# Kernel optimization log

Measured on AMD Instinct MI355X. Metric: run time of the kernel, lower is better.

## Reference

```python
import jax, jax.numpy as jnp
import numpy as np

K_LEN, I_LEN, DIM = 1024, 8192, 128


def setup_inputs() -> dict:
    key = jax.random.key(0)
    k1, k2 = jax.random.split(key)
    kernel = jax.random.normal(k1, (K_LEN, DIM), dtype=jnp.float32)
    x = jax.random.normal(k2, (I_LEN, DIM), dtype=jnp.float32)
    return {"kernel": kernel, "x": x}


def _cost_matrix(kernel, x):
    # squared Euclidean pairwise distances, (K, I), via GEMM form
    k2 = jnp.sum(kernel * kernel, axis=-1)  # (K,)
    x2 = jnp.sum(x * x, axis=-1)            # (I,)
    c = k2[:, None] + x2[None, :] - 2.0 * (kernel @ x.T)
    return jnp.maximum(c, 0.0)


def _acc_matrix(c):
    # DTW DP: D[i,j] = c[i,j] + min(D[i-1,j-1], D[i-1,j], D[i,j-1])
    # Row recurrence solved per-row with a (min,+) prefix scan:
    #   e[j] = min(D_prev[j-1], D_prev[j]) + c[j]   (e[0] = D_prev[0] + c[0])
    #   D[j] = S[j] + cummin(e - S),  S = cumsum(c_row)
    row0 = jnp.cumsum(c[0])

    def step(prev, c_row):
        m = jnp.concatenate([prev[:1], jnp.minimum(prev[:-1], prev[1:])])
        e = m + c_row
        S = jnp.cumsum(c_row)
        row = S + jax.lax.cummin(e - S)
        return row, row

    _, rows = jax.lax.scan(step, row0, c[1:])
    return jnp.concatenate([row0[None, :], rows], axis=0)  # (K, I)


def _backtrack(D):
    # tslearn-style backtracking from (K-1, I-1) to (0, 0).
    # Candidate order [diag, up, left]; argmin ties pick first (diag),
    # matching numpy.argmin used by tslearn. Out-of-range -> +inf border.
    K, I = D.shape
    Dp = jnp.full((K + 1, I + 1), jnp.inf, dtype=D.dtype).at[1:, 1:].set(D)
    L = K + I - 1  # max possible path length

    def step(carry, _):
        k, i, fin = carry
        emit = (k, i, jnp.logical_not(fin))
        fin2 = fin | ((k == 0) & (i == 0))
        cand = jnp.stack([Dp[k, i], Dp[k, i + 1], Dp[k + 1, i]])
        a = jnp.argmin(cand)
        nk = jnp.where(fin2, k, k - (a != 2).astype(k.dtype))
        ni = jnp.where(fin2, i, i - (a != 1).astype(i.dtype))
        return (nk, ni, fin2), emit

    init = (jnp.int32(K - 1), jnp.int32(I - 1), jnp.bool_(False))
    _, (ks, iss, valid) = jax.lax.scan(step, init, None, length=L)
    return ks, iss, valid


def reference(kernel, x):
    # Path search uses detached tensors in the original module.
    c = jax.lax.stop_gradient(_cost_matrix(kernel, x))
    D = _acc_matrix(c)
    ks, iss, valid = _backtrack(D)
    # sum of squared diffs along the optimal alignment path (gather + reduce)
    d2 = jnp.sum((kernel[ks] - x[iss]) ** 2, axis=-1)  # (L,)
    return jnp.sum(jnp.where(valid, d2, 0.0))
```

## Files before the change

### kernel.cpp

```cpp
#include <hip/hip_runtime.h>
#include <hip/hip_bf16.h>

typedef unsigned short ushort_t;
typedef unsigned int uint_t;

#define KL 1024
#define IL 8192
#define DIMV 128
#define NS 16
#define NB 258
#define NIT2 270
#define SSH (8256*64)
#define GATE 416
#define INF __builtin_inff()

typedef __attribute__((ext_vector_type(8))) short v8s;
typedef __attribute__((ext_vector_type(4))) float v4f;

__global__ __launch_bounds__(256) void knorms(
    const float* __restrict__ kern, const float* __restrict__ xx,
    float* __restrict__ x2, float* __restrict__ k2, int* __restrict__ flags) {
  if (blockIdx.x == 0 && threadIdx.x < NS) flags[threadIdx.x] = 0;
  const int lane = threadIdx.x & 63;
  const int row = blockIdx.x * 4 + (threadIdx.x >> 6);
  const float* src;
  float* dst;
  if (row < IL) { src = xx + (size_t)row * DIMV; dst = x2 + row; }
  else          { src = kern + (size_t)(row - IL) * DIMV; dst = k2 + (row - IL); }
  float2 v = *(const float2*)(src + lane * 2);
  float ss = v.x * v.x + v.y * v.y;
  #pragma unroll
  for (int off = 32; off > 0; off >>= 1) ss += __shfl_down(ss, off, 64);
  if (lane == 0) *dst = ss;
}

__device__ __forceinline__ v8s pack_bf16x8(float4 a, float4 b) {
  union { unsigned int u[4]; v8s v; } r;
  union { __hip_bfloat162 h; unsigned int u; } t;
  t.h = __float22bfloat162_rn(make_float2(a.x, a.y)); r.u[0] = t.u;
  t.h = __float22bfloat162_rn(make_float2(a.z, a.w)); r.u[1] = t.u;
  t.h = __float22bfloat162_rn(make_float2(b.x, b.y)); r.u[2] = t.u;
  t.h = __float22bfloat162_rn(make_float2(b.z, b.w)); r.u[3] = t.u;
  return r.v;
}

__global__ __launch_bounds__(256) void kgemm(
    const float* __restrict__ kern, const float* __restrict__ xx,
    const float* __restrict__ x2, const float* __restrict__ k2,
    ushort_t* __restrict__ c_h) {
  __shared__ float ctile[64 * 64];
  const int T = threadIdx.x;
  const int w = T >> 6;
  const int lane = T & 63;
  const int lo = lane & 15;
  const int hi = lane >> 4;
  const int i0 = blockIdx.x * 64;
  const int s  = blockIdx.y;
  const int kr0 = s * 64;

  v4f acc[4] = {};
  #pragma unroll
  for (int ks = 0; ks < 4; ks++) {
    const int k = ks * 32 + hi * 8;
    const float* bp = xx + (size_t)(i0 + w * 16 + lo) * DIMV + k;
    v8s bf = pack_bf16x8(*(const float4*)bp, *(const float4*)(bp + 4));
    #pragma unroll
    for (int rt = 0; rt < 4; rt++) {
      const float* ap = kern + (size_t)(kr0 + rt * 16 + lo) * DIMV + k;
      v8s af = pack_bf16x8(*(const float4*)ap, *(const float4*)(ap + 4));
      acc[rt] = __builtin_amdgcn_mfma_f32_16x16x32_bf16(af, bf, acc[rt], 0, 0, 0);
    }
  }
  const float x2v = x2[i0 + w * 16 + lo];
  const int n_local = w * 16 + lo;
  #pragma unroll
  for (int rt = 0; rt < 4; rt++) {
    float4 k2f = *(const float4*)&k2[kr0 + rt * 16 + hi * 4];
    #pragma unroll
    for (int q = 0; q < 4; q++) {
      const int m_local = rt * 16 + hi * 4 + q;
      float cval = fmaxf((&k2f.x)[q] + x2v - 2.f * acc[rt][q], 0.f);
      ctile[n_local * 64 + ((m_local + 2 * n_local) & 63)] = cval;
    }
  }
  __syncthreads();
  _Float16* ob = (_Float16*)(c_h + (size_t)s * SSH);
  #pragma unroll
  for (int q = 0; q < 32; q++) {
    int tt = w + q * 4;
    int di = tt - lane;
    if (tt <= 126 && di >= 0 && di < 64) {
      int t = i0 + tt;
      int tp = t >> 1;
      ob[(((size_t)(tp >> 4) * 1024) + lane * 16 + (tp & 15)) * 2 + (t & 1)] =
          (_Float16)ctile[di * 64 + ((lane + 2 * di) & 63)];
    }
  }
}

__device__ __forceinline__ float dpp_wave_shr1(float oldv, float src) {
  return __int_as_float(__builtin_amdgcn_update_dpp(
      __float_as_int(oldv), __float_as_int(src), 0x138, 0xF, 0xF, false));
}

__global__ __launch_bounds__(320, 1) void kdp(
    const ushort_t* __restrict__ c_h, float* __restrict__ bound,
    int* __restrict__ flags, float* __restrict__ out) {
  __shared__ __align__(16) float ring[4 * 4 * 32];
  __shared__ __align__(16) float feed[4 * 32];
  const int g = blockIdx.x;
  const int wv = threadIdx.x >> 6;
  const int lane = threadIdx.x & 63;
  const int sb = g * 4;

  float Dcur = INF, Dul = INF;
  int fchk = 0, fpend = 0;
  float rfeed = INF;
  const float* bin = bound + (size_t)(sb > 0 ? sb - 1 : 0) * IL;
  float* bout3 = bound + (size_t)(sb + 3) * IL;

  const uint_t* cbase = (const uint_t*)c_h +
      (size_t)(sb + (wv < 4 ? wv : 0)) * (SSH / 2) + lane * 16;

  uint_t P[16], Q[16];

  if (wv < 4) {
    const uint4* sp = (const uint4*)cbase;
    *(uint4*)&P[0] = sp[0]; *(uint4*)&P[4] = sp[1];
    *(uint4*)&P[8] = sp[2]; *(uint4*)&P[12] = sp[3];
    if (g == 0 && wv == 0 && lane == 0) Dcur = 0.f;
  } else {
    if (g > 0) {
      int f;
      do { f = __hip_atomic_load(&flags[sb - 1], __ATOMIC_RELAXED, __HIP_MEMORY_SCOPE_AGENT); } while (f < GATE);
      fchk = f; fpend = f;
      if (lane < 32) {
        feed[lane]      = __hip_atomic_load(&bin[lane],      __ATOMIC_RELAXED, __HIP_MEMORY_SCOPE_AGENT);
        feed[32 + lane] = __hip_atomic_load(&bin[32 + lane], __ATOMIC_RELAXED, __HIP_MEMORY_SCOPE_AGENT);
        rfeed           = __hip_atomic_load(&bin[64 + lane], __ATOMIC_RELAXED, __HIP_MEMORY_SCOPE_AGENT);
      }
    } else {
      if (lane < 32) { feed[lane] = INF; feed[32+lane] = INF; feed[64+lane] = INF; feed[96+lane] = INF; }
    }
  }
  __syncthreads();

  auto body = [&](int i, uint_t (&cur)[16], uint_t (&nxt)[16]) {
    if (wv < 4) {
      const int W = i - 3 * wv;
      int Wn = W + 1; Wn = Wn < 0 ? 0 : (Wn > NB - 1 ? NB - 1 : Wn);
      {
        const uint4* sp = (const uint4*)(cbase + (size_t)Wn * 1024);
        *(uint4*)&nxt[0]  = sp[0]; *(uint4*)&nxt[4]  = sp[1];
        *(uint4*)&nxt[8]  = sp[2]; *(uint4*)&nxt[12] = sp[3];
      }
      if (W >= 0 && W < NB) {
        const float* fb = (wv == 0) ? &feed[(W & 3) * 32]
                                    : &ring[(wv - 1) * 128 + (W & 3) * 32];
        float fv[32];
        #pragma unroll
        for (int q = 0; q < 8; q++) {
          float4 f4 = *(const float4*)(fb + q * 4);
          fv[4 * q]     = f4.x; fv[4 * q + 1] = f4.y;
          fv[4 * q + 2] = f4.z; fv[4 * q + 3] = f4.w;
        }
        #pragma unroll
        for (int tt = 0; tt < 32; tt++) asm("" : "+v"(fv[tt]));
        float cvv[32];
        #pragma unroll
        for (int tp = 0; tp < 16; tp++) {
          union { uint_t u; _Float16 h[2]; } cu; cu.u = cur[tp];
          cvv[2 * tp]     = (float)cu.h[0];
          cvv[2 * tp + 1] = (float)cu.h[1];
        }
        #pragma unroll
        for (int tt = 0; tt < 32; tt++) asm("" : "+v"(cvv[tt]));
        float bb[32];
        if (W >= 2 && W < 256) {
          #pragma unroll
          for (int tt = 0; tt < 32; tt++) {
            float Dup = dpp_wave_shr1(fv[tt], Dcur);
            float m1 = fminf(Dul, Dcur);
            Dcur = cvv[tt] + fminf(m1, Dup);
            Dul = Dup;
            bb[tt] = Dcur;
          }
        } else {
          const int t0 = W * 32;
          #pragma unroll
          for (int tt = 0; tt < 32; tt++) {
            const int t = t0 + tt;
            float Dup = dpp_wave_shr1(fv[tt], Dcur);
            float m1 = fminf(Dul, Dcur);
            float Dnew = cvv[tt] + fminf(m1, Dup);
            const bool alo = (t >= lane);
            const bool ahi = (t - lane < IL);
            if (alo) Dul = Dup;
            if (alo && ahi) Dcur = Dnew;
            bb[tt] = Dcur;
          }
        }
        if (lane == 63) {
          const int base2 = wv * 128 + (((W - 2) & 3) << 5);
          const int base1 = wv * 128 + (((W - 1) & 3) << 5);
          if (W >= 2) {
            #pragma unroll
            for (int tt = 0; tt < 31; tt++) ring[base2 + tt + 1] = bb[tt];
          }
          if (W >= 1) ring[base1] = bb[31];
        }
      }
      asm volatile("s_waitcnt lgkmcnt(0)" ::: "memory");
      __builtin_amdgcn_s_barrier();
    } else {
      asm volatile("s_waitcnt vmcnt(0)" ::: "memory");
      if (g > 0) {
        if (fpend > fchk) fchk = fpend;
        const int Fw = i + 2;
        if (Fw >= 2 && Fw <= 255 && lane < 32) feed[(Fw & 3) * 32 + lane] = rfeed;
        const int Fl = i + 3;
        if (Fl <= 255) {
          const int need = 32 * (Fl + 1);
          if (fchk < need) {
            int f;
            do { f = __hip_atomic_load(&flags[sb - 1], __ATOMIC_RELAXED, __HIP_MEMORY_SCOPE_AGENT); } while (f < need);
            fchk = f;
          }
          if (lane < 32)
            rfeed = __hip_atomic_load(&bin[32 * Fl + lane], __ATOMIC_RELAXED, __HIP_MEMORY_SCOPE_AGENT);
        }
        fpend = __hip_atomic_load(&flags[sb - 1], __ATOMIC_RELAXED, __HIP_MEMORY_SCOPE_AGENT);
      }
      if (g < 3) {
        const int E = i - 12;
        if (E >= 0 && E < 256 && lane < 32) {
          float bv2 = ring[3 * 128 + (E & 3) * 32 + lane];
          __hip_atomic_store(&bout3[32 * E + lane], bv2, __ATOMIC_RELAXED, __HIP_MEMORY_SCOPE_AGENT);
        }
        const int Ep = i - 13;
        if (Ep >= 0 && Ep < 256 && lane == 0)
          __hip_atomic_store(&flags[sb + 3], 32 * Ep + 32, __ATOMIC_RELAXED, __HIP_MEMORY_SCOPE_AGENT);
      }
      asm volatile("s_waitcnt lgkmcnt(0)" ::: "memory");
      __builtin_amdgcn_s_barrier();
    }
  };

  for (int i = 0; i < NIT2; i += 2) {
    body(i, P, Q);
    body(i + 1, Q, P);
  }

  asm volatile("s_waitcnt vmcnt(0)" ::: "memory");
  if (g == 3 && wv == 3 && lane == 63) out[0] = Dcur;
}

extern "C" void kernel_launch(void* const* d_in, const int* in_sizes, int n_in,
                              void* d_out, int out_size, void* d_ws, size_t ws_size,
                              hipStream_t stream) {
  const float* kern = (const float*)d_in[0];
  const float* xx   = (const float*)d_in[1];
  char* ws = (char*)d_ws;
  const size_t OFF_X2 = (size_t)NS * SSH * 2;
  const size_t OFF_K2 = OFF_X2 + (size_t)IL * 4;
  const size_t OFF_BD = OFF_K2 + (size_t)KL * 4;
  const size_t OFF_FL = OFF_BD + (size_t)NS * IL * 4;
  ushort_t* c_h  = (ushort_t*)ws;
  float* x2    = (float*)(ws + OFF_X2);
  float* k2    = (float*)(ws + OFF_K2);
  float* bnd   = (float*)(ws + OFF_BD);
  int*   flags = (int*)(ws + OFF_FL);

  knorms<<<(IL + KL) / 4, 256, 0, stream>>>(kern, xx, x2, k2, flags);
  kgemm<<<dim3(IL / 64, NS), 256, 0, stream>>>(kern, xx, x2, k2, c_h);
  kdp<<<4, 320, 0, stream>>>(c_h, bnd, flags, (float*)d_out);
}
```

Measured before the change: 453.2 us.

## Unroll DTW wavefront recurrence two steps per iteration to shorten dependency chain

Result: slower. 688.0 us (+51.8%).

```diff
diff --git a/kernel.cpp b/kernel.cpp
--- a/kernel.cpp
+++ b/kernel.cpp
@@ -102,6 +102,9 @@
   return __int_as_float(__builtin_amdgcn_update_dpp(
       __float_as_int(oldv), __float_as_int(src), 0x138, 0xF, 0xF, false));
 }
+__device__ __forceinline__ float bperm_f(int idx_bytes, float v) {
+  return __int_as_float(__builtin_amdgcn_ds_bpermute(idx_bytes, __float_as_int(v)));
+}
 
 __global__ __launch_bounds__(320, 1) void kdp(
     const ushort_t* __restrict__ c_h, float* __restrict__ bound,
@@ -113,11 +116,12 @@
   const int lane = threadIdx.x & 63;
   const int sb = g * 4;
 
-  float Dcur = INF, Dul = INF;
+  float X = INF, y1 = INF, y2 = INF;
   int fchk = 0, fpend = 0;
   float rfeed = INF;
   const float* bin = bound + (size_t)(sb > 0 ? sb - 1 : 0) * IL;
   float* bout3 = bound + (size_t)(sb + 3) * IL;
+  const int bpi2 = ((lane - 2) & 63) << 2;
 
   const uint_t* cbase = (const uint_t*)c_h +
       (size_t)(sb + (wv < 4 ? wv : 0)) * (SSH / 2) + lane * 16;
@@ -128,7 +132,7 @@
     const uint4* sp = (const uint4*)cbase;
     *(uint4*)&P[0] = sp[0]; *(uint4*)&P[4] = sp[1];
     *(uint4*)&P[8] = sp[2]; *(uint4*)&P[12] = sp[3];
-    if (g == 0 && wv == 0 && lane == 0) Dcur = 0.f;
+    if (g == 0 && wv == 0 && lane == 0) X = 0.f;
   } else {
     if (g > 0) {
       int f;
@@ -164,8 +168,6 @@
           fv[4 * q]     = f4.x; fv[4 * q + 1] = f4.y;
           fv[4 * q + 2] = f4.z; fv[4 * q + 3] = f4.w;
         }
-        #pragma unroll
-        for (int tt = 0; tt < 32; tt++) asm("" : "+v"(fv[tt]));
         float cvv[32];
         #pragma unroll
         for (int tp = 0; tp < 16; tp++) {
@@ -173,32 +175,42 @@
           cvv[2 * tp]     = (float)cu.h[0];
           cvv[2 * tp + 1] = (float)cu.h[1];
         }
-        #pragma unroll
-        for (int tt = 0; tt < 32; tt++) asm("" : "+v"(cvv[tt]));
         float bb[32];
         if (W >= 2 && W < 256) {
+          float cs[16];
           #pragma unroll
-          for (int tt = 0; tt < 32; tt++) {
-            float Dup = dpp_wave_shr1(fv[tt], Dcur);
-            float m1 = fminf(Dul, Dcur);
-            Dcur = cvv[tt] + fminf(m1, Dup);
-            Dul = Dup;
-            bb[tt] = Dcur;
+          for (int p = 0; p < 16; p++) cs[p] = dpp_wave_shr1(cvv[2 * p], cvv[2 * p]);
+          #pragma unroll
+          for (int p = 0; p < 16; p++) {
+            const int u = 2 * p;
+            float x1 = dpp_wave_shr1(fv[u], X);
+            float x2 = bperm_f(bpi2, X);
+            x2 = (lane < 2) ? fv[u] : x2;
+            float Du = cvv[u] + fminf(fminf(X, x1), y1);
+            float E  = cs[p] + fminf(fminf(x1, y2), x2);
+            E = (lane == 0) ? fv[u + 1] : E;
+            float Du1 = cvv[u + 1] + fminf(fminf(Du, x1), E);
+            float z1 = dpp_wave_shr1(fv[u + 1], Du);
+            float z2 = bperm_f(bpi2, Du);
+            z2 = (lane < 2) ? fv[u + 1] : z2;
+            bb[u] = Du; bb[u + 1] = Du1;
+            X = Du1; y1 = z1; y2 = z2;
           }
         } else {
           const int t0 = W * 32;
           #pragma unroll
           for (int tt = 0; tt < 32; tt++) {
             const int t = t0 + tt;
-            float Dup = dpp_wave_shr1(fv[tt], Dcur);
-            float m1 = fminf(Dul, Dcur);
+            float Dup = dpp_wave_shr1(fv[tt], X);
+            float m1 = fminf(y1, X);
             float Dnew = cvv[tt] + fminf(m1, Dup);
             const bool alo = (t >= lane);
             const bool ahi = (t - lane < IL);
-            if (alo) Dul = Dup;
-            if (alo && ahi) Dcur = Dnew;
-            bb[tt] = Dcur;
-          }
+            if (alo) y1 = Dup;
+            if (alo && ahi) X = Dnew;
+            bb[tt] = X;
+          }
+          y2 = dpp_wave_shr1(y1, y1);
         }
         if (lane == 63) {
           const int base2 = wv * 128 + (((W - 2) & 3) << 5);
@@ -252,7 +264,7 @@
   }
 
   asm volatile("s_waitcnt vmcnt(0)" ::: "memory");
-  if (g == 3 && wv == 3 && lane == 63) out[0] = Dcur;
+  if (g == 3 && wv == 3 && lane == 63) out[0] = X;
 }
 
 extern "C" void kernel_launch(void* const* d_in, const int* in_sizes, int n_in,
```
